# Performance work log

Measured on AMD Instinct MI355X. Metric: run time of the kernel, lower is better.

The kernel has to match this reference:

```python
import jax, jax.numpy as jnp
import numpy as np

B, S, D, H = 2, 2048, 1024, 16
HD = D // H                 # head_dim = 64
BLOCK = 16                  # _DEFAULT_BLOCK_SIZE
NB = S // BLOCK             # max_blocks_per_seq = 128
WINDOW = 512
NEG = jnp.float32(-1e30)


def setup_inputs() -> dict:
    key = jax.random.key(0)
    ks = jax.random.split(key, 5)
    x = jax.random.normal(ks[0], (B, S, D), jnp.float32)
    scale = D ** -0.5
    wq = jax.random.normal(ks[1], (D, D), jnp.float32) * scale
    wk = jax.random.normal(ks[2], (D, D), jnp.float32) * scale
    wv = jax.random.normal(ks[3], (D, D), jnp.float32) * scale
    wo = jax.random.normal(ks[4], (D, D), jnp.float32) * scale
    # sequential paged layout (matches the module's synthesized-cache fallback)
    block_tables = jnp.arange(B * NB, dtype=jnp.int32).reshape(B, NB)
    slot_mapping = jnp.arange(B * S, dtype=jnp.int32)
    context_lens = jnp.full((B,), S, dtype=jnp.int32)
    return {"x": x, "wq": wq, "wk": wk, "wv": wv, "wo": wo,
            "block_tables": block_tables, "slot_mapping": slot_mapping,
            "context_lens": context_lens, "window_size": WINDOW}


def reference(x, wq, wk, wv, wo, block_tables, slot_mapping, context_lens, window_size):
    b, s, d = x.shape
    # Q/K/V projections (nn.Linear, bias=False: y = x @ W^T)
    q = (x @ wq.T).reshape(b, s, H, HD)
    k = (x @ wk.T).reshape(b, s, H, HD)
    v = (x @ wv.T).reshape(b, s, H, HD)

    # ---- memopt_C.write_cache: scatter K/V into the physical slot pool ----
    num_slots = b * s
    key_cache = jnp.zeros((num_slots, H, HD), x.dtype).at[slot_mapping].set(k.reshape(-1, H, HD))
    value_cache = jnp.zeros((num_slots, H, HD), x.dtype).at[slot_mapping].set(v.reshape(-1, H, HD))

    # ---- dynamic_sparse_attention: read KV through block_tables ----
    t = jnp.arange(s)
    # physical slot of logical token t of sequence b: block_tables[b, t//BLOCK]*BLOCK + t%BLOCK
    slots = block_tables[:, t // BLOCK].astype(jnp.int32) * BLOCK + (t % BLOCK)[None, :].astype(jnp.int32)  # [B,S]
    kc = key_cache[slots]    # [B,S,H,HD]
    vc = value_cache[slots]  # [B,S,H,HD]

    scores = jnp.einsum('bqhd,bkhd->bhqk', q, kc) * (HD ** -0.5)  # [B,H,S,S]
    qpos = t[:, None]
    kpos = t[None, :]
    # causal + window-limited visibility (window_size tokens of history)
    vis = (kpos <= qpos) & (qpos - kpos < window_size)            # [S,S]
    ctx = t[None, :] < context_lens[:, None]                       # [B,S]
    mask = vis[None, None, :, :] & ctx[:, None, None, :]
    scores = jnp.where(mask, scores, NEG)
    attn = jax.nn.softmax(scores, axis=-1)
    out = jnp.einsum('bhqk,bkhd->bqhd', attn, vc).reshape(b, s, d)
    return out @ wo.T
```

## Files before the change

kernel.cpp:

```cpp
#include <hip/hip_runtime.h>

typedef __attribute__((ext_vector_type(4))) float  f32x4;
typedef __attribute__((ext_vector_type(8))) short  bf16x8;

typedef __attribute__((address_space(3))) void lds_void_t;
typedef __attribute__((address_space(1))) void g_void_t;

#define S_LEN  2048
#define DMODEL 1024
#define NHEAD  16
#define HDIM   64
#define NBLK   128
#define BATCH  2
#define KT     64
#define VP     72

__device__ __forceinline__ short f2bf(float f) {
  union { float f; unsigned u; } v; v.f = f;
  unsigned r = v.u + 0x7fffu + ((v.u >> 16) & 1u);
  return (short)(r >> 16);
}

__global__ __launch_bounds__(256) void cvt_all_kernel(
    const float* __restrict__ x,  const float* __restrict__ wq,
    const float* __restrict__ wk, const float* __restrict__ wv,
    const float* __restrict__ wo,
    short* __restrict__ xb,  short* __restrict__ wqb,
    short* __restrict__ wkb, short* __restrict__ wvb,
    short* __restrict__ wob) {
  const long i = ((long)blockIdx.x * 256 + threadIdx.x) * 8;
  const float* s; short* d; long off;
  if (i < 4194304L)      { s = x;  d = xb;  off = i; }
  else if (i < 5242880L) { s = wq; d = wqb; off = i - 4194304L; }
  else if (i < 6291456L) { s = wk; d = wkb; off = i - 5242880L; }
  else if (i < 7340032L) { s = wv; d = wvb; off = i - 6291456L; }
  else                   { s = wo; d = wob; off = i - 7340032L; }
  f32x4 a = *(const f32x4*)(s + off);
  f32x4 b = *(const f32x4*)(s + off + 4);
  bf16x8 o;
  o[0]=f2bf(a[0]); o[1]=f2bf(a[1]); o[2]=f2bf(a[2]); o[3]=f2bf(a[3]);
  o[4]=f2bf(b[0]); o[5]=f2bf(b[1]); o[6]=f2bf(b[2]); o[7]=f2bf(b[3]);
  *(bf16x8*)(d + off) = o;
}

__global__ __launch_bounds__(512, 2) void gemm8_kernel(
    const short* __restrict__ A,
    const short* __restrict__ W0, const short* __restrict__ W1, const short* __restrict__ W2,
    const int* __restrict__ slot_map,
    short* __restrict__ qbuf, short* __restrict__ kcache, short* __restrict__ vcache)
{
  extern __shared__ short smem[];

  const int m0 = blockIdx.x * 256;
  const int n0 = blockIdx.y * 256;
  const int wsel = n0 >> 10;
  const short* W = (wsel == 0) ? W0 : (wsel == 1) ? W1 : W2;
  const short* Ag = A + (size_t)m0 * DMODEL;
  const short* Bg = W + (size_t)(n0 & 1023) * DMODEL;

  const int tid  = threadIdx.x;
  const int wave = tid >> 6, lane = tid & 63;
  const int l15 = lane & 15, lg = lane >> 4;
  const int wr = wave >> 2, wc = wave & 3;
  const int swz = l15 & 7;

  short* const A0 = smem;
  short* const B0 = smem + 16384;
  short* const A1 = smem + 32768;
  short* const B1 = smem + 49152;

  f32x4 acc[8][4];
#pragma unroll
  for (int m = 0; m < 8; m++)
#pragma unroll
    for (int n = 0; n < 4; n++) acc[m][n] = (f32x4)0.f;

#define STAGE_HALF(DST, SRCBASE, K0)                                                      \
  { _Pragma("unroll")                                                                     \
    for (int p = 0; p < 4; ++p) {                                                         \
      const int gidx = p * 512 + tid;                                                     \
      const int r = gidx >> 3;                                                            \
      const int cs = (gidx & 7) ^ (r & 7);                                                \
      __builtin_amdgcn_global_load_lds((g_void_t*)((SRCBASE) + (size_t)r * DMODEL + (K0) + cs * 8), \
                                       (lds_void_t*)((DST) + (p * 512 + wave * 64) * 8), 16, 0, 0); \
    } }

#define PHASE_SYNC() do {                                       \
    asm volatile("" ::: "memory");                              \
    __builtin_amdgcn_s_barrier();                               \
    asm volatile("s_waitcnt lgkmcnt(0)" ::: "memory");          \
    __builtin_amdgcn_sched_barrier(0);                          \
  } while (0)

#define PHASE_END() do {                                        \
    asm volatile("" ::: "memory");                              \
    __builtin_amdgcn_s_barrier();                               \
    asm volatile("" ::: "memory");                              \
  } while (0)

  STAGE_HALF(A0, Ag, 0);
  STAGE_HALF(B0, Bg, 0);
  asm volatile("s_waitcnt vmcnt(0)" ::: "memory");
  __builtin_amdgcn_s_barrier();
  asm volatile("" ::: "memory");

  const int NT = DMODEL / 64;
  for (int t = 0; t < NT; ++t) {
    const int cur = t & 1;
    short* const As_ = cur ? A1 : A0;
    short* const Bs_ = cur ? B1 : B0;
    short* const An_ = cur ? A0 : A1;
    short* const Bn_ = cur ? B0 : B1;
    const int kn = (t + 1) * 64;

    bf16x8 af0[4][2], af1[4][2], bf0[2][2], bf1[2][2];

#pragma unroll
    for (int m4 = 0; m4 < 4; ++m4) {
      const int row = wr * 128 + m4 * 16 + l15;
#pragma unroll
      for (int ks = 0; ks < 2; ++ks)
        af0[m4][ks] = *(const bf16x8*)(As_ + row * 64 + (((ks * 4 + lg) ^ swz) << 3));
    }
#pragma unroll
    for (int n2 = 0; n2 < 2; ++n2) {
      const int row = wc * 64 + n2 * 16 + l15;
#pragma unroll
      for (int ks = 0; ks < 2; ++ks)
        bf0[n2][ks] = *(const bf16x8*)(Bs_ + row * 64 + (((ks * 4 + lg) ^ swz) << 3));
    }
    if (t + 1 < NT) { STAGE_HALF(An_, Ag, kn); }
    PHASE_SYNC();
    __builtin_amdgcn_s_setprio(1);
#pragma unroll
    for (int m4 = 0; m4 < 4; ++m4)
#pragma unroll
      for (int n2 = 0; n2 < 2; ++n2)
#pragma unroll
        for (int ks = 0; ks < 2; ++ks)
          acc[m4][n2] = __builtin_amdgcn_mfma_f32_16x16x32_bf16(af0[m4][ks], bf0[n2][ks], acc[m4][n2], 0, 0, 0);
    __builtin_amdgcn_s_setprio(0);
    PHASE_END();

#pragma unroll
    for (int n2 = 0; n2 < 2; ++n2) {
      const int row = wc * 64 + 32 + n2 * 16 + l15;
#pragma unroll
      for (int ks = 0; ks < 2; ++ks)
        bf1[n2][ks] = *(const bf16x8*)(Bs_ + row * 64 + (((ks * 4 + lg) ^ swz) << 3));
    }
    if (t + 1 < NT) { STAGE_HALF(Bn_, Bg, kn); }
    PHASE_SYNC();
    __builtin_amdgcn_s_setprio(1);
#pragma unroll
    for (int m4 = 0; m4 < 4; ++m4)
#pragma unroll
      for (int n2 = 0; n2 < 2; ++n2)
#pragma unroll
        for (int ks = 0; ks < 2; ++ks)
          acc[m4][2 + n2] = __builtin_amdgcn_mfma_f32_16x16x32_bf16(af0[m4][ks], bf1[n2][ks], acc[m4][2 + n2], 0, 0, 0);
    __builtin_amdgcn_s_setprio(0);
    PHASE_END();

#pragma unroll
    for (int m4 = 0; m4 < 4; ++m4) {
      const int row = wr * 128 + 64 + m4 * 16 + l15;
#pragma unroll
      for (int ks = 0; ks < 2; ++ks)
        af1[m4][ks] = *(const bf16x8*)(As_ + row * 64 + (((ks * 4 + lg) ^ swz) << 3));
    }
    PHASE_SYNC();
    __builtin_amdgcn_s_setprio(1);
#pragma unroll
    for (int m4 = 0; m4 < 4; ++m4)
#pragma unroll
      for (int n2 = 0; n2 < 2; ++n2)
#pragma unroll
        for (int ks = 0; ks < 2; ++ks)
          acc[4 + m4][n2] = __builtin_amdgcn_mfma_f32_16x16x32_bf16(af1[m4][ks], bf0[n2][ks], acc[4 + m4][n2], 0, 0, 0);
    __builtin_amdgcn_s_setprio(0);
    PHASE_END();

    __builtin_amdgcn_s_setprio(1);
#pragma unroll
    for (int m4 = 0; m4 < 4; ++m4)
#pragma unroll
      for (int n2 = 0; n2 < 2; ++n2)
#pragma unroll
        for (int ks = 0; ks < 2; ++ks)
          acc[4 + m4][2 + n2] = __builtin_amdgcn_mfma_f32_16x16x32_bf16(af1[m4][ks], bf1[n2][ks], acc[4 + m4][2 + n2], 0, 0, 0);
    __builtin_amdgcn_s_setprio(0);
    asm volatile("s_waitcnt vmcnt(0)" ::: "memory");
    PHASE_END();
  }
#undef STAGE_HALF
#undef PHASE_SYNC
#undef PHASE_END

  const int ncol0 = (n0 & 1023) + wc * 64;
#pragma unroll
  for (int mf = 0; mf < 8; ++mf) {
    const int rowb = m0 + wr * 128 + mf * 16 + lg * 4;
#pragma unroll
    for (int r = 0; r < 4; ++r) {
      const int row = rowb + r;
      short* dst;
      if (wsel == 0) {
        dst = qbuf + (size_t)row * DMODEL + ncol0;
      } else {
        const int slot = slot_map[row];
        dst = ((wsel == 1) ? kcache : vcache) + (size_t)slot * DMODEL + ncol0;
      }
#pragma unroll
      for (int nf = 0; nf < 4; ++nf) dst[nf * 16 + l15] = f2bf(acc[mf][nf][r]);
    }
  }
}

template<int MODE>
__global__ __launch_bounds__(256) void gemm_kernel(
    const short* __restrict__ A,
    const short* __restrict__ W0, const short* __restrict__ W1, const short* __restrict__ W2,
    const int* __restrict__ slot_map,
    short* __restrict__ qbuf, short* __restrict__ kcache, short* __restrict__ vcache,
    float* __restrict__ outf)
{
  __shared__ short As[128 * 32];
  __shared__ short Bs[128 * 32];

  const int m0 = blockIdx.x * 128;
  const int n0 = blockIdx.y * 128;

  const short* Bg;
  if (MODE == 0) {
    const int wsel = n0 >> 10;
    const short* w = (wsel == 0) ? W0 : (wsel == 1) ? W1 : W2;
    Bg = w + (n0 & 1023) * DMODEL;
  } else {
    Bg = W0 + n0 * DMODEL;
  }
  const short* Ag = A + (size_t)m0 * DMODEL;

  const int tid  = threadIdx.x;
  const int wave = tid >> 6, lane = tid & 63;
  const int wr = wave >> 1, wc = wave & 1;
  const int l15 = lane & 15, lg = lane >> 4;

  f32x4 acc[4][4];
#pragma unroll
  for (int m = 0; m < 4; m++)
#pragma unroll
    for (int n = 0; n < 4; n++) acc[m][n] = (f32x4)0.f;

  for (int k0 = 0; k0 < DMODEL; k0 += 32) {
    __syncthreads();
#pragma unroll
    for (int i = 0; i < 2; i++) {
      const int e = i * 256 + tid;
      const int r = e >> 2;
      const int c = (e & 3) << 3;
      const short* ga = Ag + r * DMODEL + k0 + c;
      const short* gb = Bg + r * DMODEL + k0 + c;
      const int ldso = (i * 256 + wave * 64) * 8;
      __builtin_amdgcn_global_load_lds((g_void_t*)(ga), (lds_void_t*)(As + ldso), 16, 0, 0);
      __builtin_amdgcn_global_load_lds((g_void_t*)(gb), (lds_void_t*)(Bs + ldso), 16, 0, 0);
    }
    __syncthreads();

    bf16x8 af[4], bfr[4];
#pragma unroll
    for (int m = 0; m < 4; m++)
      af[m] = *(const bf16x8*)(As + (wr * 64 + m * 16 + l15) * 32 + lg * 8);
#pragma unroll
    for (int n = 0; n < 4; n++)
      bfr[n] = *(const bf16x8*)(Bs + (wc * 64 + n * 16 + l15) * 32 + lg * 8);
#pragma unroll
    for (int m = 0; m < 4; m++)
#pragma unroll
      for (int n = 0; n < 4; n++)
        acc[m][n] = __builtin_amdgcn_mfma_f32_16x16x32_bf16(af[m], bfr[n], acc[m][n], 0, 0, 0);
  }

#pragma unroll
  for (int m = 0; m < 4; m++) {
    const int rowb = m0 + wr * 64 + m * 16 + lg * 4;
#pragma unroll
    for (int n = 0; n < 4; n++) {
      const int col = n0 + wc * 64 + n * 16 + l15;
#pragma unroll
      for (int r = 0; r < 4; r++) {
        const int rw = rowb + r;
        const float val = acc[m][n][r];
        if (MODE == 1) {
          outf[(size_t)rw * DMODEL + col] = val;
        } else {
          const short bv = f2bf(val);
          if (col < DMODEL) {
            qbuf[(size_t)rw * DMODEL + col] = bv;
          } else {
            const int slot = slot_map[rw];
            if (col < 2 * DMODEL)
              kcache[(size_t)slot * DMODEL + (col - DMODEL)] = bv;
            else
              vcache[(size_t)slot * DMODEL + (col - 2 * DMODEL)] = bv;
          }
        }
      }
    }
  }
}

__global__ __launch_bounds__(512, 4) void attn_kernel(
    const short* __restrict__ qbuf,
    const short* __restrict__ kcache, const short* __restrict__ vcache,
    const int* __restrict__ block_tables, const int* __restrict__ context_lens,
    const int* __restrict__ window_size,
    short* __restrict__ attn_out)
{
  __shared__ short Ks[KT * 64];
  __shared__ short Vt[HDIM * VP];
  __shared__ short Pb[8 * 16 * VP];

  const int b = blockIdx.z, h = blockIdx.y, q0 = blockIdx.x * 128;
  const int ctx = context_lens[b];
  const int ws  = window_size[0];
  const int* bt = block_tables + b * NBLK;

  const int tid  = threadIdx.x;
  const int wave = tid >> 6, lane = tid & 63;
  const int l15 = lane & 15, lg = lane >> 4;
  const int qw = q0 + wave * 16;

  const short* qp = qbuf + ((size_t)(b * S_LEN + qw + l15)) * DMODEL + h * HDIM;
  const bf16x8 qf0 = *(const bf16x8*)(qp + lg * 8);
  const bf16x8 qf1 = *(const bf16x8*)(qp + 32 + lg * 8);

  f32x4 oacc[4];
  float lrow[4];
#pragma unroll
  for (int i = 0; i < 4; i++) { oacc[i] = (f32x4)0.f; lrow[i] = 0.f; }

  int kstart = q0 - ws + 1; if (kstart < 0) kstart = 0; kstart &= ~(KT - 1);
  int kend = q0 + 128; if (kend > ctx) kend = ctx;

  const int kr = tid >> 3;
  const int dc = (tid & 7) << 3;
  const float rscale = 0.125f;
  const float FM = 12.f;
  short* pw = Pb + wave * (16 * VP);
  const int swz = (l15 & 7) << 4;

  bf16x8 kreg = (bf16x8)0, vreg = (bf16x8)0;
  {
    const int key = kstart + kr;
    if (key < ctx) {
      const int slot = bt[key >> 4] * 16 + (key & 15);
      kreg = *(const bf16x8*)(kcache + (size_t)slot * DMODEL + h * HDIM + dc);
      vreg = *(const bf16x8*)(vcache + (size_t)slot * DMODEL + h * HDIM + dc);
    }
  }

  for (int kt = kstart; kt < kend; kt += KT) {
    __syncthreads();
    *(bf16x8*)((char*)Ks + kr * 128 + ((dc * 2) ^ ((kr & 7) << 4))) = kreg;
    const int vcol = (kr + dc) & 63;
#pragma unroll
    for (int j = 0; j < 8; j++) Vt[(dc + j) * VP + vcol] = vreg[j];
    kreg = (bf16x8)0; vreg = (bf16x8)0;
    if (kt + KT < kend) {
      const int key = kt + KT + kr;
      if (key < ctx) {
        const int slot = bt[key >> 4] * 16 + (key & 15);
        kreg = *(const bf16x8*)(kcache + (size_t)slot * DMODEL + h * HDIM + dc);
        vreg = *(const bf16x8*)(vcache + (size_t)slot * DMODEL + h * HDIM + dc);
      }
    }
    __syncthreads();

    if ((kt > qw + 15) || (kt + (KT - 1) <= qw - ws)) continue;

    f32x4 sacc[4];
#pragma unroll
    for (int cg = 0; cg < 4; cg++) sacc[cg] = (f32x4)0.f;
#pragma unroll
    for (int cg = 0; cg < 4; cg++) {
      const char* kp = (const char*)Ks + (cg * 16 + l15) * 128;
      const bf16x8 k0 = *(const bf16x8*)(kp + ((lg * 16) ^ swz));
      const bf16x8 k1 = *(const bf16x8*)(kp + ((64 + lg * 16) ^ swz));
      sacc[cg] = __builtin_amdgcn_mfma_f32_16x16x32_bf16(qf0, k0, sacc[cg], 0, 0, 0);
      sacc[cg] = __builtin_amdgcn_mfma_f32_16x16x32_bf16(qf1, k1, sacc[cg], 0, 0, 0);
    }

    const bool fullvis = (kt + (KT - 1) <= qw) && (qw + 15 - kt < ws) && (kt + (KT - 1) < ctx);

    if (fullvis) {
#pragma unroll
      for (int r = 0; r < 4; r++) {
        const float e0 = __expf(sacc[0][r] * rscale - FM);
        const float e1 = __expf(sacc[1][r] * rscale - FM);
        const float e2 = __expf(sacc[2][r] * rscale - FM);
        const float e3 = __expf(sacc[3][r] * rscale - FM);
        lrow[r] += (e0 + e1) + (e2 + e3);
        short* pr = pw + (lg * 4 + r) * VP + l15;
        pr[0]  = f2bf(e0); pr[16] = f2bf(e1);
        pr[32] = f2bf(e2); pr[48] = f2bf(e3);
      }
    } else {
#pragma unroll
      for (int r = 0; r < 4; r++) {
        const int qrow = qw + lg * 4 + r;
        const int key0 = kt + l15;
        const bool ok0 = (key0      <= qrow) && (qrow - key0      < ws) && (key0      < ctx);
        const bool ok1 = (key0 + 16 <= qrow) && (qrow - key0 - 16 < ws) && (key0 + 16 < ctx);
        const bool ok2 = (key0 + 32 <= qrow) && (qrow - key0 - 32 < ws) && (key0 + 32 < ctx);
        const bool ok3 = (key0 + 48 <= qrow) && (qrow - key0 - 48 < ws) && (key0 + 48 < ctx);
        const float e0 = ok0 ? __expf(sacc[0][r] * rscale - FM) : 0.f;
        const float e1 = ok1 ? __expf(sacc[1][r] * rscale - FM) : 0.f;
        const float e2 = ok2 ? __expf(sacc[2][r] * rscale - FM) : 0.f;
        const float e3 = ok3 ? __expf(sacc[3][r] * rscale - FM) : 0.f;
        lrow[r] += (e0 + e1) + (e2 + e3);
        short* pr = pw + (lg * 4 + r) * VP + l15;
        pr[0]  = f2bf(e0); pr[16] = f2bf(e1);
        pr[32] = f2bf(e2); pr[48] = f2bf(e3);
      }
    }

    asm volatile("s_waitcnt lgkmcnt(0)" ::: "memory");

#pragma unroll
    for (int kk = 0; kk < 2; kk++) {
      const bf16x8 pa = *(const bf16x8*)(pw + l15 * VP + kk * 32 + lg * 8);
#pragma unroll
      for (int dn = 0; dn < 4; dn++) {
        const int vrow = dn * 16 + l15;
        const int roff = (kk * 32 + lg * 8 + (vrow & ~7)) & 63;
        const bf16x8 vb = *(const bf16x8*)(Vt + vrow * VP + roff);
        oacc[dn] = __builtin_amdgcn_mfma_f32_16x16x32_bf16(pa, vb, oacc[dn], 0, 0, 0);
      }
    }
  }

#pragma unroll
  for (int r = 0; r < 4; r++) {
    float ls = lrow[r];
    ls += __shfl_xor(ls, 1); ls += __shfl_xor(ls, 2);
    ls += __shfl_xor(ls, 4); ls += __shfl_xor(ls, 8);
    const float inv = 1.f / fmaxf(ls, 1e-30f);
    const int row = qw + lg * 4 + r;
    short* op = attn_out + ((size_t)(b * S_LEN + row)) * DMODEL + h * HDIM;
#pragma unroll
    for (int dn = 0; dn < 4; dn++)
      op[dn * 16 + l15] = f2bf(oacc[dn][r] * inv);
  }
}

extern "C" void kernel_launch(void* const* d_in, const int* in_sizes, int n_in,
                              void* d_out, int out_size, void* d_ws, size_t ws_size,
                              hipStream_t stream) {
  const float* x  = (const float*)d_in[0];
  const float* wq = (const float*)d_in[1];
  const float* wk = (const float*)d_in[2];
  const float* wv = (const float*)d_in[3];
  const float* wo = (const float*)d_in[4];
  const int* block_tables = (const int*)d_in[5];
  const int* slot_mapping = (const int*)d_in[6];
  const int* context_lens = (const int*)d_in[7];
  const int* window_size  = (const int*)d_in[8];
  float* out = (float*)d_out;

  char* ws = (char*)d_ws;
  short* xb     = (short*)(ws + (size_t)( 0 << 20));
  short* wqb    = (short*)(ws + (size_t)( 8 << 20));
  short* wkb    = (short*)(ws + (size_t)(10 << 20));
  short* wvb    = (short*)(ws + (size_t)(12 << 20));
  short* wob    = (short*)(ws + (size_t)(14 << 20));
  short* qbuf   = (short*)(ws + (size_t)(16 << 20));
  short* kcache = (short*)(ws + (size_t)(24 << 20));
  short* vcache = (short*)(ws + (size_t)(32 << 20));
  short* abuf   = (short*)(ws + (size_t)(40 << 20));

  static bool gemm8_init = [] {
    hipFuncSetAttribute(reinterpret_cast<const void*>(&gemm8_kernel),
                        hipFuncAttributeMaxDynamicSharedMemorySize, 131072);
    return true;
  }();
  (void)gemm8_init;

  cvt_all_kernel<<<4096, 256, 0, stream>>>(x, wq, wk, wv, wo, xb, wqb, wkb, wvb, wob);

  gemm8_kernel<<<dim3(16, 12), 512, 131072, stream>>>(xb, wqb, wkb, wvb, slot_mapping,
                                                      qbuf, kcache, vcache);

  attn_kernel<<<dim3(S_LEN / 128, NHEAD, BATCH), 512, 0, stream>>>(
      qbuf, kcache, vcache, block_tables, context_lens, window_size, abuf);

  gemm_kernel<1><<<dim3(32, 8), 256, 0, stream>>>(abuf, wob, nullptr, nullptr, nullptr,
                                                  nullptr, nullptr, nullptr, out);
}
```

Baseline: 100.4 us.

## Retile fused QKV GEMM to 256x192 tiles with four-phase pipelined staging

Changes the fused QKV projection GEMM tile from 256x256 to 256x192, so the grid grows from 192 to 256 workgroups. That count matches the CU count of the device, which improves wave balance. B tiles can now straddle the Q/K/V weight boundaries, so weight selection and output routing become per-row and per-column. The K-loop is restructured into four phases, each loading a quarter of A and all three B fragments, with finer-grained vmcnt waits that overlap the next tile's loads with MFMA work. LDS use drops to 112 KB. The trade-off is per-element branching in staging and epilogue, plus lower arithmetic intensity per tile.

```diff
diff --git a/kernel.cpp b/kernel.cpp
--- a/kernel.cpp
+++ b/kernel.cpp
@@ -52,11 +52,8 @@
   extern __shared__ short smem[];
 
   const int m0 = blockIdx.x * 256;
-  const int n0 = blockIdx.y * 256;
-  const int wsel = n0 >> 10;
-  const short* W = (wsel == 0) ? W0 : (wsel == 1) ? W1 : W2;
+  const int n0 = blockIdx.y * 192;
   const short* Ag = A + (size_t)m0 * DMODEL;
-  const short* Bg = W + (size_t)(n0 & 1023) * DMODEL;
 
   const int tid  = threadIdx.x;
   const int wave = tid >> 6, lane = tid & 63;
@@ -64,26 +61,32 @@
   const int wr = wave >> 2, wc = wave & 3;
   const int swz = l15 & 7;
 
-  short* const A0 = smem;
-  short* const B0 = smem + 16384;
-  short* const A1 = smem + 32768;
-  short* const B1 = smem + 49152;
-
-  f32x4 acc[8][4];
+  short* const A0s = smem;
+  short* const B0s = smem + 16384;
+  short* const A1s = smem + 28672;
+  short* const B1s = smem + 45056;
+
+  f32x4 acc[8][3];
 #pragma unroll
   for (int m = 0; m < 8; m++)
 #pragma unroll
-    for (int n = 0; n < 4; n++) acc[m][n] = (f32x4)0.f;
-
-#define STAGE_HALF(DST, SRCBASE, K0)                                                      \
-  { _Pragma("unroll")                                                                     \
-    for (int p = 0; p < 4; ++p) {                                                         \
-      const int gidx = p * 512 + tid;                                                     \
-      const int r = gidx >> 3;                                                            \
-      const int cs = (gidx & 7) ^ (r & 7);                                                \
-      __builtin_amdgcn_global_load_lds((g_void_t*)((SRCBASE) + (size_t)r * DMODEL + (K0) + cs * 8), \
-                                       (lds_void_t*)((DST) + (p * 512 + wave * 64) * 8), 16, 0, 0); \
-    } }
+    for (int n = 0; n < 3; n++) acc[m][n] = (f32x4)0.f;
+
+#define STAGE_A(DST, K0, P) {                                                              \
+    const int gidx = (P) * 512 + tid;                                                      \
+    const int r = gidx >> 3;                                                               \
+    const int cs = (gidx & 7) ^ (r & 7);                                                   \
+    __builtin_amdgcn_global_load_lds((g_void_t*)(Ag + (size_t)r * DMODEL + (K0) + cs * 8), \
+        (lds_void_t*)((DST) + ((P) * 512 + wave * 64) * 8), 16, 0, 0); }
+
+#define STAGE_B(DST, K0, P) {                                                              \
+    const int gidx = (P) * 512 + tid;                                                      \
+    const int r = gidx >> 3;                                                               \
+    const int grow = n0 + r;                                                               \
+    const short* wb = (grow < 1024) ? W0 : (grow < 2048) ? W1 : W2;                        \
+    const int cs = (gidx & 7) ^ (r & 7);                                                   \
+    __builtin_amdgcn_global_load_lds((g_void_t*)(wb + (size_t)(grow & 1023) * DMODEL + (K0) + cs * 8), \
+        (lds_void_t*)((DST) + ((P) * 512 + wave * 64) * 8), 16, 0, 0); }
 
 #define PHASE_SYNC() do {                                       \
     asm volatile("" ::: "memory");                              \
@@ -98,121 +101,99 @@
     asm volatile("" ::: "memory");                              \
   } while (0)
 
-  STAGE_HALF(A0, Ag, 0);
-  STAGE_HALF(B0, Bg, 0);
+#define PHASE_READ_A(BUF, Q)                                                               \
+    _Pragma("unroll") for (int mi = 0; mi < 2; ++mi) {                                     \
+      const int row = wr * 128 + ((Q) * 2 + mi) * 16 + l15;                                \
+      _Pragma("unroll") for (int ks = 0; ks < 2; ++ks)                                     \
+        af[mi][ks] = *(const bf16x8*)((BUF) + row * 64 + (((ks * 4 + lg) ^ swz) << 3)); }
+
+#define PHASE_MFMA(Q)                                                                      \
+    __builtin_amdgcn_s_setprio(1);                                                         \
+    _Pragma("unroll") for (int mi = 0; mi < 2; ++mi)                                       \
+    _Pragma("unroll") for (int nt = 0; nt < 3; ++nt)                                       \
+    _Pragma("unroll") for (int ks = 0; ks < 2; ++ks)                                       \
+      acc[(Q) * 2 + mi][nt] = __builtin_amdgcn_mfma_f32_16x16x32_bf16(                     \
+          af[mi][ks], bfr[nt][ks], acc[(Q) * 2 + mi][nt], 0, 0, 0);                        \
+    __builtin_amdgcn_s_setprio(0);
+
+  STAGE_B(B0s, 0, 0); STAGE_B(B0s, 0, 1); STAGE_B(B0s, 0, 2);
+  STAGE_A(A0s, 0, 0); STAGE_A(A0s, 0, 2); STAGE_A(A0s, 0, 1); STAGE_A(A0s, 0, 3);
   asm volatile("s_waitcnt vmcnt(0)" ::: "memory");
   __builtin_amdgcn_s_barrier();
   asm volatile("" ::: "memory");
 
   const int NT = DMODEL / 64;
   for (int t = 0; t < NT; ++t) {
-    const int cur = t & 1;
-    short* const As_ = cur ? A1 : A0;
-    short* const Bs_ = cur ? B1 : B0;
-    short* const An_ = cur ? A0 : A1;
-    short* const Bn_ = cur ? B0 : B1;
+    const bool stg = (t + 1 < NT);
+    short* const Ac = (t & 1) ? A1s : A0s;
+    short* const Bc = (t & 1) ? B1s : B0s;
+    short* const An = (t & 1) ? A0s : A1s;
+    short* const Bn = (t & 1) ? B0s : B1s;
     const int kn = (t + 1) * 64;
 
-    bf16x8 af0[4][2], af1[4][2], bf0[2][2], bf1[2][2];
-
-#pragma unroll
-    for (int m4 = 0; m4 < 4; ++m4) {
-      const int row = wr * 128 + m4 * 16 + l15;
+    bf16x8 af[2][2], bfr[3][2];
+
+#pragma unroll
+    for (int nt = 0; nt < 3; ++nt) {
+      const int row = wc * 48 + nt * 16 + l15;
 #pragma unroll
       for (int ks = 0; ks < 2; ++ks)
-        af0[m4][ks] = *(const bf16x8*)(As_ + row * 64 + (((ks * 4 + lg) ^ swz) << 3));
-    }
-#pragma unroll
-    for (int n2 = 0; n2 < 2; ++n2) {
-      const int row = wc * 64 + n2 * 16 + l15;
-#pragma unroll
-      for (int ks = 0; ks < 2; ++ks)
-        bf0[n2][ks] = *(const bf16x8*)(Bs_ + row * 64 + (((ks * 4 + lg) ^ swz) << 3));
-    }
-    if (t + 1 < NT) { STAGE_HALF(An_, Ag, kn); }
+        bfr[nt][ks] = *(const bf16x8*)(Bc + row * 64 + (((ks * 4 + lg) ^ swz) << 3));
+    }
+    PHASE_READ_A(Ac, 0);
+    if (stg) { STAGE_B(Bn, kn, 0); STAGE_B(Bn, kn, 1); STAGE_B(Bn, kn, 2); }
     PHASE_SYNC();
-    __builtin_amdgcn_s_setprio(1);
-#pragma unroll
-    for (int m4 = 0; m4 < 4; ++m4)
-#pragma unroll
-      for (int n2 = 0; n2 < 2; ++n2)
-#pragma unroll
-        for (int ks = 0; ks < 2; ++ks)
-          acc[m4][n2] = __builtin_amdgcn_mfma_f32_16x16x32_bf16(af0[m4][ks], bf0[n2][ks], acc[m4][n2], 0, 0, 0);
-    __builtin_amdgcn_s_setprio(0);
+    PHASE_MFMA(0);
     PHASE_END();
 
-#pragma unroll
-    for (int n2 = 0; n2 < 2; ++n2) {
-      const int row = wc * 64 + 32 + n2 * 16 + l15;
-#pragma unroll
-      for (int ks = 0; ks < 2; ++ks)
-        bf1[n2][ks] = *(const bf16x8*)(Bs_ + row * 64 + (((ks * 4 + lg) ^ swz) << 3));
-    }
-    if (t + 1 < NT) { STAGE_HALF(Bn_, Bg, kn); }
+    PHASE_READ_A(Ac, 1);
+    if (stg) { STAGE_A(An, kn, 0); STAGE_A(An, kn, 2); }
     PHASE_SYNC();
-    __builtin_amdgcn_s_setprio(1);
-#pragma unroll
-    for (int m4 = 0; m4 < 4; ++m4)
-#pragma unroll
-      for (int n2 = 0; n2 < 2; ++n2)
-#pragma unroll
-        for (int ks = 0; ks < 2; ++ks)
-          acc[m4][2 + n2] = __builtin_amdgcn_mfma_f32_16x16x32_bf16(af0[m4][ks], bf1[n2][ks], acc[m4][2 + n2], 0, 0, 0);
-    __builtin_amdgcn_s_setprio(0);
+    PHASE_MFMA(1);
+    if (stg) { asm volatile("s_waitcnt vmcnt(6)" ::: "memory"); }
+    else     { asm volatile("s_waitcnt vmcnt(1)" ::: "memory"); }
     PHASE_END();
 
-#pragma unroll
-    for (int m4 = 0; m4 < 4; ++m4) {
-      const int row = wr * 128 + 64 + m4 * 16 + l15;
-#pragma unroll
-      for (int ks = 0; ks < 2; ++ks)
-        af1[m4][ks] = *(const bf16x8*)(As_ + row * 64 + (((ks * 4 + lg) ^ swz) << 3));
-    }
+    PHASE_READ_A(Ac, 2);
+    if (stg) { STAGE_A(An, kn, 1); }
     PHASE_SYNC();
-    __builtin_amdgcn_s_setprio(1);
-#pragma unroll
-    for (int m4 = 0; m4 < 4; ++m4)
-#pragma unroll
-      for (int n2 = 0; n2 < 2; ++n2)
-#pragma unroll
-        for (int ks = 0; ks < 2; ++ks)
-          acc[4 + m4][n2] = __builtin_amdgcn_mfma_f32_16x16x32_bf16(af1[m4][ks], bf0[n2][ks], acc[4 + m4][n2], 0, 0, 0);
-    __builtin_amdgcn_s_setprio(0);
+    PHASE_MFMA(2);
+    if (stg) { asm volatile("s_waitcnt vmcnt(6)" ::: "memory"); }
+    else     { asm volatile("s_waitcnt vmcnt(0)" ::: "memory"); }
     PHASE_END();
 
-    __builtin_amdgcn_s_setprio(1);
-#pragma unroll
-    for (int m4 = 0; m4 < 4; ++m4)
-#pragma unroll
-      for (int n2 = 0; n2 < 2; ++n2)
-#pragma unroll
-        for (int ks = 0; ks < 2; ++ks)
-          acc[4 + m4][2 + n2] = __builtin_amdgcn_mfma_f32_16x16x32_bf16(af1[m4][ks], bf1[n2][ks], acc[4 + m4][2 + n2], 0, 0, 0);
-    __builtin_amdgcn_s_setprio(0);
-    asm volatile("s_waitcnt vmcnt(0)" ::: "memory");
+    PHASE_READ_A(Ac, 3);
+    if (stg) { STAGE_A(An, kn, 3); }
+    PHASE_SYNC();
+    PHASE_MFMA(3);
+    asm volatile("s_waitcnt vmcnt(2)" ::: "memory");
     PHASE_END();
   }
-#undef STAGE_HALF
+#undef STAGE_A
+#undef STAGE_B
 #undef PHASE_SYNC
 #undef PHASE_END
-
-  const int ncol0 = (n0 & 1023) + wc * 64;
+#undef PHASE_READ_A
+#undef PHASE_MFMA
+
 #pragma unroll
   for (int mf = 0; mf < 8; ++mf) {
     const int rowb = m0 + wr * 128 + mf * 16 + lg * 4;
 #pragma unroll
-    for (int r = 0; r < 4; ++r) {
-      const int row = rowb + r;
-      short* dst;
-      if (wsel == 0) {
-        dst = qbuf + (size_t)row * DMODEL + ncol0;
-      } else {
-        const int slot = slot_map[row];
-        dst = ((wsel == 1) ? kcache : vcache) + (size_t)slot * DMODEL + ncol0;
-      }
-#pragma unroll
-      for (int nf = 0; nf < 4; ++nf) dst[nf * 16 + l15] = f2bf(acc[mf][nf][r]);
+    for (int r4 = 0; r4 < 4; ++r4) {
+      const int row = rowb + r4;
+      const int slot = slot_map[row];
+#pragma unroll
+      for (int nt = 0; nt < 3; ++nt) {
+        const int col = n0 + wc * 48 + nt * 16 + l15;
+        const short bv = f2bf(acc[mf][nt][r4]);
+        if (col < DMODEL)
+          qbuf[(size_t)row * DMODEL + col] = bv;
+        else if (col < 2 * DMODEL)
+          kcache[(size_t)slot * DMODEL + (col - DMODEL)] = bv;
+        else
+          vcache[(size_t)slot * DMODEL + (col - 2 * DMODEL)] = bv;
+      }
     }
   }
 }
@@ -481,14 +462,14 @@
 
   static bool gemm8_init = [] {
     hipFuncSetAttribute(reinterpret_cast<const void*>(&gemm8_kernel),
-                        hipFuncAttributeMaxDynamicSharedMemorySize, 131072);
+                        hipFuncAttributeMaxDynamicSharedMemorySize, 114688);
     return true;
   }();
   (void)gemm8_init;
 
   cvt_all_kernel<<<4096, 256, 0, stream>>>(x, wq, wk, wv, wo, xb, wqb, wkb, wvb, wob);
 
-  gemm8_kernel<<<dim3(16, 12), 512, 131072, stream>>>(xb, wqb, wkb, wvb, slot_mapping,
+  gemm8_kernel<<<dim3(16, 16), 512, 114688, stream>>>(xb, wqb, wkb, wvb, slot_mapping,
                                                       qbuf, kcache, vcache);
 
   attn_kernel<<<dim3(S_LEN / 128, NHEAD, BATCH), 512, 0, stream>>>(
```

New measurement: 98.95 us. Within noise of the previous version (-1.5%).
